# Optimization experiments

Hardware: AMD Instinct MI355X
Metric: run time of the kernel (lower is better)

## Reference

```python
import jax, jax.numpy as jnp
import numpy as np

HEAD_SIZE = 64
EMB_SIZE = 1024
B, T = 8, 2048


def setup_inputs() -> dict:
    key = jax.random.key(0)
    k_x, k_q, k_k, k_v, k_m = jax.random.split(key, 5)
    X = jax.random.normal(k_x, (B, T, EMB_SIZE), dtype=jnp.float32)
    # nn.Linear(emb, head, bias=False) weights have shape (head, emb)
    s = EMB_SIZE ** -0.5
    Wq = jax.random.uniform(k_q, (HEAD_SIZE, EMB_SIZE), jnp.float32, -s, s)
    Wk = jax.random.uniform(k_k, (HEAD_SIZE, EMB_SIZE), jnp.float32, -s, s)
    Wv = jax.random.uniform(k_v, (HEAD_SIZE, EMB_SIZE), jnp.float32, -s, s)
    padding_mask = jax.random.randint(k_m, (B, T), 0, 2).astype(bool)
    # ensure no row is fully masked (would yield NaN softmax)
    padding_mask = padding_mask.at[:, 0].set(False)
    return {"X": X, "Wq": Wq, "Wk": Wk, "Wv": Wv, "padding_mask": padding_mask}


def reference(X, Wq, Wk, Wv, padding_mask):
    # X: (B,T,C); W*: (H,C); padding_mask: (B,T) bool, True = masked key
    C = X.shape[-1]
    Q = jnp.einsum('btc,hc->bth', X, Wq)
    K = jnp.einsum('btc,hc->bth', X, Wk)
    V = jnp.einsum('btc,hc->bth', X, Wv)
    # NOTE: source scales by emb_size**-0.5 (C), not head_size**-0.5
    wei = jnp.einsum('bth,bsh->bts', Q, K) * (C ** -0.5)  # (B,T,T)
    wei = jnp.where(padding_mask[:, None, :], -jnp.inf, wei)
    wei = jax.nn.softmax(wei, axis=-1)  # dropout disabled (eval mode)
    out = jnp.einsum('bts,bsh->bth', wei, V)  # (B,T,H)
    return out
```

## Files before the change

kernel.cpp:

```cpp
#include <hip/hip_runtime.h>
#include <hip/hip_bf16.h>
#include <math.h>


#define T_SEQ 2048
#define EMB 1024
#define HS 64
#define NB 8

typedef __attribute__((ext_vector_type(8))) short short8;
typedef __attribute__((ext_vector_type(4))) float f32x4;
typedef __attribute__((ext_vector_type(2))) unsigned int uint2_t;
typedef unsigned short ushort_t;

static __device__ inline ushort_t f2bf(float f) {
  union { float f; unsigned u; } v; v.f = f;
  unsigned r = v.u + 0x7FFF + ((v.u >> 16) & 1);
  return (ushort_t)(r >> 16);
}
static __device__ inline unsigned pk2(float a, float b) {
  return (unsigned)f2bf(a) | ((unsigned)f2bf(b) << 16);
}
static __device__ inline void lds_barrier() {
  asm volatile("s_waitcnt lgkmcnt(0)" ::: "memory");
  __builtin_amdgcn_s_barrier();
}

__global__ __launch_bounds__(256) void convw_kernel(
    const float* __restrict__ Wq, const float* __restrict__ Wk,
    const float* __restrict__ Wv, ushort_t* __restrict__ Wb) {
  const int m = blockIdx.x >> 4;
  const int blk = blockIdx.x & 15;
  const float* src = (m == 0) ? Wq : (m == 1) ? Wk : Wv;
  const float scale = (m == 0) ? 0.03125f : 1.0f;
  const int base = blk * 4096 + threadIdx.x * 16;
  ushort_t* dst = Wb + m * 65536;
  ushort_t tmp[16];
#pragma unroll
  for (int j = 0; j < 4; ++j) {
    float4 x = *(const float4*)(src + base + j * 4);
    tmp[j * 4 + 0] = f2bf(x.x * scale);
    tmp[j * 4 + 1] = f2bf(x.y * scale);
    tmp[j * 4 + 2] = f2bf(x.z * scale);
    tmp[j * 4 + 3] = f2bf(x.w * scale);
  }
  *(short8*)(dst + base) = *(short8*)tmp;
  *(short8*)(dst + base + 8) = *(short8*)(tmp + 8);
}

__global__ __launch_bounds__(256) void proj_kernel(
    const float* __restrict__ X, const ushort_t* __restrict__ Wb,
    ushort_t* __restrict__ Qb, ushort_t* __restrict__ Kb,
    ushort_t* __restrict__ Vtb) {
  __shared__ __align__(16) ushort_t Xs[2][64 * 128];
  const int tid = threadIdx.x;
  const int lane = tid & 63, w = tid >> 6;
  const int l15 = lane & 15, hi = lane >> 4;
  const long rbase = (long)blockIdx.x * 64;

  const ushort_t* Wrow[3];
#pragma unroll
  for (int t = 0; t < 3; ++t) {
    const int ht = 3 * w + t, m = ht >> 2, hs = ht & 3;
    Wrow[t] = Wb + m * 65536 + (hs * 16 + l15) * 1024 + hi * 8;
  }

  short8 wfA[6], wfB[6], wfC[6], wfD[6];
  auto loadw = [&](short8 (&dst)[6], int s) {
#pragma unroll
    for (int t = 0; t < 3; ++t) {
      dst[2 * t + 0] = *(const short8*)(Wrow[t] + s * 64);
      dst[2 * t + 1] = *(const short8*)(Wrow[t] + s * 64 + 32);
    }
  };
  loadw(wfA, 0); loadw(wfB, 1); loadw(wfC, 2);

  float4 xrA[8], xrB[8];
  auto stage_load = [&](float4 (&xr)[8], int c) {
#pragma unroll
    for (int j = 0; j < 8; ++j) {
      const int F = j * 256 + tid;
      const int row = F >> 5, c4 = F & 31;
      xr[j] = *(const float4*)(X + (rbase + row) * EMB + c * 128 + c4 * 4);
    }
  };
  auto stage_write = [&](float4 (&xr)[8], int buf) {
    ushort_t* Xd = Xs[buf];
#pragma unroll
    for (int j = 0; j < 8; ++j) {
      const int F = j * 256 + tid;
      const int row = F >> 5, c4 = F & 31;
      uint2_t pv;
      pv.x = pk2(xr[j].x, xr[j].y);
      pv.y = pk2(xr[j].z, xr[j].w);
      *(uint2_t*)((char*)(Xd + row * 128) + ((c4 * 8) ^ ((row & 7) << 4))) = pv;
    }
  };

  f32x4 acc[4][3];
#pragma unroll
  for (int rt = 0; rt < 4; ++rt)
#pragma unroll
    for (int t = 0; t < 3; ++t) acc[rt][t] = (f32x4){0.f, 0.f, 0.f, 0.f};

  const int swA = (l15 & 7) << 4;

  auto body = [&](int s, int buf, short8 (&cur)[6], short8 (&pre)[6]) {
    if (s + 3 < 16) loadw(pre, s + 3);
    const int sb = (s & 1) * 128;
#pragma unroll
    for (int rt = 0; rt < 4; ++rt) {
      const char* rowp = (const char*)(Xs[buf] + (rt * 16 + l15) * 128);
      short8 a0 = *(const short8*)(rowp + ((sb + hi * 16) ^ swA));
      short8 a1 = *(const short8*)(rowp + ((sb + 64 + hi * 16) ^ swA));
#pragma unroll
      for (int t = 0; t < 3; ++t) {
        acc[rt][t] = __builtin_amdgcn_mfma_f32_16x16x32_bf16(
            a0, cur[2 * t + 0], acc[rt][t], 0, 0, 0);
        acc[rt][t] = __builtin_amdgcn_mfma_f32_16x16x32_bf16(
            a1, cur[2 * t + 1], acc[rt][t], 0, 0, 0);
      }
    }
  };

  stage_load(xrA, 0);
  stage_write(xrA, 0);
  stage_load(xrB, 1);
  lds_barrier();

  stage_load(xrA, 2);
  body(0, 0, wfA, wfD); body(1, 0, wfB, wfA);
  stage_write(xrB, 1); lds_barrier();
  stage_load(xrB, 3);
  body(2, 1, wfC, wfB); body(3, 1, wfD, wfC);
  stage_write(xrA, 0); lds_barrier();
  stage_load(xrA, 4);
  body(4, 0, wfA, wfD); body(5, 0, wfB, wfA);
  stage_write(xrB, 1); lds_barrier();
  stage_load(xrB, 5);
  body(6, 1, wfC, wfB); body(7, 1, wfD, wfC);
  stage_write(xrA, 0); lds_barrier();
  stage_load(xrA, 6);
  body(8, 0, wfA, wfD); body(9, 0, wfB, wfA);
  stage_write(xrB, 1); lds_barrier();
  stage_load(xrB, 7);
  body(10, 1, wfC, wfB); body(11, 1, wfD, wfC);
  stage_write(xrA, 0); lds_barrier();
  body(12, 0, wfA, wfD); body(13, 0, wfB, wfA);
  stage_write(xrB, 1); lds_barrier();
  body(14, 1, wfC, wfB); body(15, 1, wfD, wfC);

  const long bblk = rbase >> 11;
  const long tb0 = rbase & 2047;
  ushort_t* outs[2] = {Qb, Kb};
#pragma unroll
  for (int rt = 0; rt < 4; ++rt)
#pragma unroll
    for (int t = 0; t < 3; ++t) {
      const int ht = 3 * w + t, m = ht >> 2, hs = ht & 3;
      const int h = hs * 16 + l15;
      if (m < 2) {
#pragma unroll
        for (int r = 0; r < 4; ++r) {
          const long row = rbase + rt * 16 + 4 * hi + r;
          outs[m][row * 64 + h] = f2bf(acc[rt][t][r]);
        }
      } else {
        const long tloc = tb0 + rt * 16 + 4 * hi;
        uint2_t v;
        v.x = pk2(acc[rt][t][0], acc[rt][t][1]);
        v.y = pk2(acc[rt][t][2], acc[rt][t][3]);
        *(uint2_t*)(Vtb + bblk * (long)HS * T_SEQ + (long)h * T_SEQ + tloc) = v;
      }
    }
}

__global__ __launch_bounds__(512) void attn_kernel(
    const ushort_t* __restrict__ Qb, const ushort_t* __restrict__ Kb,
    const ushort_t* __restrict__ Vtb, const int* __restrict__ mask,
    float* __restrict__ out) {
  __shared__ __align__(16) char Lds[152064];

  const int tid = threadIdx.x;
  const int lane = tid & 63, w = tid >> 6;
  const int l15 = lane & 15, hi = lane >> 4;
  const int qs = w & 3, g = w >> 2;
  const int si = tid & 255;
  const int id = blockIdx.x;
  const int b = id & 7;
  const int q0 = (id >> 3) * 64;

  ushort_t* biasB = (ushort_t*)(Lds + 147456);
  float* alphaArr = (float*)(Lds + 151552);

  {
    const ushort_t nb = f2bf(-1e30f);
    const int* mp = mask + b * T_SEQ + tid * 4;
    int4 m0 = *(const int4*)(mp);
    ushort_t t4[4];
    t4[0] = m0.x ? nb : 0; t4[1] = m0.y ? nb : 0;
    t4[2] = m0.z ? nb : 0; t4[3] = m0.w ? nb : 0;
    *(uint2_t*)(biasB + tid * 4) = *(uint2_t*)t4;
  }

  const ushort_t* Qrow = Qb + (long)(b * T_SEQ + q0 + qs * 16 + l15) * 64;
  const short8 qf0 = *(const short8*)(Qrow + hi * 8);
  const short8 qf1 = *(const short8*)(Qrow + 32 + hi * 8);

  const ushort_t* Kg = Kb + (long)b * T_SEQ * 64;
  const ushort_t* Vg = Vtb + (long)b * HS * T_SEQ;

  short8 kregA[2], vregA[2], kregB[2], vregB[2];
  auto stage_load = [&](short8 (&kreg)[2], short8 (&vreg)[2], int t) {
    const ushort_t* ktile = Kg + (g * 1024 + t * 64) * 64;
#pragma unroll
    for (int j = 0; j < 2; ++j)
      kreg[j] = *(const short8*)(ktile + (j * 32 + (si >> 3)) * 64 + (si & 7) * 8);
    const ushort_t* vtile = Vg + (long)(si >> 2) * T_SEQ + g * 1024 + t * 64;
#pragma unroll
    for (int j = 0; j < 2; ++j)
      vreg[j] = *(const short8*)(vtile + (si & 3) * 8 + j * 32);
  };
  auto stage_write = [&](short8 (&kreg)[2], short8 (&vreg)[2], int buf) {
    char* Kd = Lds + (g * 4 + buf) * 8192;
#pragma unroll
    for (int j = 0; j < 2; ++j) {
      const int row = j * 32 + (si >> 3);
      *(short8*)(Kd + row * 128 + (((si & 7) * 16) ^ ((row & 7) << 4))) = kreg[j];
    }
    char* Vd = Lds + 65536 + (g * 4 + buf) * 8192;
    const int vrow = si >> 2, sv = (vrow & 7) << 4;
#pragma unroll
    for (int j = 0; j < 2; ++j)
      *(short8*)(Vd + vrow * 128 + ((((si & 3) * 16) + j * 64) ^ sv)) = vreg[j];
  };

  f32x4 O[4];
#pragma unroll
  for (int ht = 0; ht < 4; ++ht) O[ht] = (f32x4){0.f, 0.f, 0.f, 0.f};
  float mrow = -1e30f, lsum = 0.f;

  char* prow = Lds + 131072 + w * 2048 + l15 * 128;
  const int sw = (l15 & 7) << 4;
  const int swr = (l15 & 7) << 4;

  auto tile_compute = [&](int t, int buf) {
    f32x4 s[4];
    const char* Kl = Lds + (g * 4 + buf) * 8192;
    __builtin_amdgcn_s_setprio(1);
#pragma unroll
    for (int kt = 0; kt < 4; ++kt) {
      const char* kr = Kl + (kt * 16 + l15) * 128;
      short8 k0 = *(const short8*)(kr + ((hi * 16) ^ swr));
      short8 k1 = *(const short8*)(kr + ((64 + hi * 16) ^ swr));
      f32x4 z = {0.f, 0.f, 0.f, 0.f};
      s[kt] = __builtin_amdgcn_mfma_f32_16x16x32_bf16(k0, qf0, z, 0, 0, 0);
      s[kt] = __builtin_amdgcn_mfma_f32_16x16x32_bf16(k1, qf1, s[kt], 0, 0, 0);
    }
    __builtin_amdgcn_s_setprio(0);

    const ushort_t* blp = biasB + g * 1024 + t * 64;
#pragma unroll
    for (int kt = 0; kt < 4; ++kt) {
      const uint2_t bu = *(const uint2_t*)(blp + kt * 16 + hi * 4);
      union { unsigned u; float f; } c0, c1, c2, c3;
      c0.u = bu.x << 16; c1.u = bu.x & 0xFFFF0000u;
      c2.u = bu.y << 16; c3.u = bu.y & 0xFFFF0000u;
      s[kt][0] += c0.f; s[kt][1] += c1.f;
      s[kt][2] += c2.f; s[kt][3] += c3.f;
    }

    float t0m = fmaxf(fmaxf(s[0][0], s[0][1]), fmaxf(s[0][2], s[0][3]));
    float t1m = fmaxf(fmaxf(s[1][0], s[1][1]), fmaxf(s[1][2], s[1][3]));
    float t2m = fmaxf(fmaxf(s[2][0], s[2][1]), fmaxf(s[2][2], s[2][3]));
    float t3m = fmaxf(fmaxf(s[3][0], s[3][1]), fmaxf(s[3][2], s[3][3]));
    float mt = fmaxf(fmaxf(t0m, t1m), fmaxf(t2m, t3m));
    mt = fmaxf(mt, __shfl_xor(mt, 16, 64));
    mt = fmaxf(mt, __shfl_xor(mt, 32, 64));

    const bool skip = __all(mt <= mrow + 8.0f);
    float mnew = mrow;
    if (!skip) {
      mnew = fmaxf(mrow, mt);
      const float alpha = __expf(mrow - mnew);
      if (lane < 16) alphaArr[w * 16 + l15] = alpha;
      lsum *= alpha;
      mrow = mnew;
    }

    float psum = 0.f;
#pragma unroll
    for (int kt = 0; kt < 4; ++kt) {
      const float p0 = __expf(s[kt][0] - mnew);
      const float p1 = __expf(s[kt][1] - mnew);
      const float p2 = __expf(s[kt][2] - mnew);
      const float p3 = __expf(s[kt][3] - mnew);
      psum += (p0 + p1) + (p2 + p3);
      const int a0 = (kt * 32 + hi * 8) ^ sw;
      *(unsigned*)(prow + a0) = pk2(p0, p1);
      *(unsigned*)(prow + a0 + 4) = pk2(p2, p3);
    }
    lsum += psum;

    if (!skip) {
      const f32x4 av = *(const f32x4*)(alphaArr + w * 16 + 4 * hi);
#pragma unroll
      for (int ht = 0; ht < 4; ++ht) O[ht] *= av;
    }

    short8 pa0 = *(const short8*)(prow + ((hi * 16) ^ sw));
    short8 pa1 = *(const short8*)(prow + ((64 + hi * 16) ^ sw));
    const char* Vl = Lds + 65536 + (g * 4 + buf) * 8192;
    __builtin_amdgcn_s_setprio(1);
#pragma unroll
    for (int ht = 0; ht < 4; ++ht) {
      const char* vr = Vl + (ht * 16 + l15) * 128;
      short8 v0 = *(const short8*)(vr + ((hi * 16) ^ swr));
      short8 v1 = *(const short8*)(vr + ((64 + hi * 16) ^ swr));
      O[ht] = __builtin_amdgcn_mfma_f32_16x16x32_bf16(pa0, v0, O[ht], 0, 0, 0);
      O[ht] = __builtin_amdgcn_mfma_f32_16x16x32_bf16(pa1, v1, O[ht], 0, 0, 0);
    }
    __builtin_amdgcn_s_setprio(0);
  };

  stage_load(kregA, vregA, 0);
  stage_load(kregB, vregB, 1);
  stage_write(kregA, vregA, 0);
  stage_write(kregB, vregB, 1);
  lds_barrier();

#pragma unroll 1
  for (int ts = 0; ts < 16; ts += 2) {
    if (ts + 2 < 16) {
      stage_load(kregA, vregA, ts + 2);
      stage_load(kregB, vregB, ts + 3);
    }
    tile_compute(ts, ts & 3);
    tile_compute(ts + 1, (ts + 1) & 3);
    if (ts + 2 < 16) {
      stage_write(kregA, vregA, (ts + 2) & 3);
      stage_write(kregB, vregB, (ts + 3) & 3);
    }
    lds_barrier();
  }

  lsum += __shfl_xor(lsum, 16, 64);
  lsum += __shfl_xor(lsum, 32, 64);

  float* mergeF = (float*)Lds;
  if (g == 1) {
    float* ml = mergeF + (qs * 64 + lane) * 18;
    ml[0] = mrow; ml[1] = lsum;
#pragma unroll
    for (int ht = 0; ht < 4; ++ht)
#pragma unroll
      for (int r = 0; r < 4; ++r) ml[2 + ht * 4 + r] = O[ht][r];
  }
  lds_barrier();
  if (g == 0) {
    const float* ml = mergeF + (qs * 64 + lane) * 18;
    const float mB = ml[0], lB = ml[1];
    const float mn = fmaxf(mrow, mB);
    const float aa = __expf(mrow - mn);
    const float ab = __expf(mB - mn);
    const float inv = 1.0f / (lsum * aa + lB * ab);
    float* ob = out + (long)(b * T_SEQ + q0 + qs * 16) * 64;
#pragma unroll
    for (int r = 0; r < 4; ++r) {
      const float aar = __shfl(aa, 4 * hi + r, 64);
      const float abr = __shfl(ab, 4 * hi + r, 64);
      const float invr = __shfl(inv, 4 * hi + r, 64);
#pragma unroll
      for (int ht = 0; ht < 4; ++ht)
        ob[(4 * hi + r) * 64 + ht * 16 + l15] =
            (O[ht][r] * aar + ml[2 + ht * 4 + r] * abr) * invr;
    }
  }
}

extern "C" void kernel_launch(void* const* d_in, const int* in_sizes, int n_in,
                              void* d_out, int out_size, void* d_ws, size_t ws_size,
                              hipStream_t stream) {
  const float* X  = (const float*)d_in[0];
  const float* Wq = (const float*)d_in[1];
  const float* Wk = (const float*)d_in[2];
  const float* Wv = (const float*)d_in[3];
  const int* mask = (const int*)d_in[4];
  float* outp = (float*)d_out;

  const long NT = (long)NB * T_SEQ * HS;
  ushort_t* wsb = (ushort_t*)d_ws;
  ushort_t* Qb  = wsb;
  ushort_t* Kb  = wsb + NT;
  ushort_t* Vtb = wsb + 2 * NT;
  ushort_t* Wb  = wsb + 3 * NT;

  convw_kernel<<<48, 256, 0, stream>>>(Wq, Wk, Wv, Wb);
  proj_kernel<<<(NB * T_SEQ) / 64, 256, 0, stream>>>(X, Wb, Qb, Kb, Vtb);
  attn_kernel<<<256, 512, 0, stream>>>(Qb, Kb, Vtb, mask, outp);
}
```

Baseline: 54.39 us.

## Stage K/V tiles via direct global-to-LDS loads and use exp2 softmax

Replaces the register-staged K/V tile loads and LDS writes with global_load_lds direct-to-LDS transfers, applying the XOR swizzle on the global address side so the LDS layout is unchanged. This frees VGPRs and removes the separate LDS write pass. Separately, log2(e) is folded into the Q weight scale so the softmax uses exp2f instead of __expf, with the rescale-skip threshold adjusted to match. Barriers become __syncthreads, which relies on the compiler inserting the vmcnt waits the async LDS loads need.

```diff
diff --git a/kernel.cpp b/kernel.cpp
--- a/kernel.cpp
+++ b/kernel.cpp
@@ -25,6 +25,11 @@
   asm volatile("s_waitcnt lgkmcnt(0)" ::: "memory");
   __builtin_amdgcn_s_barrier();
 }
+
+#define GL16(gp, lp)                                                 \
+  __builtin_amdgcn_global_load_lds(                                  \
+      (const __attribute__((address_space(1))) void*)(gp),           \
+      (__attribute__((address_space(3))) void*)(lp), 16, 0, 0)
 
 __global__ __launch_bounds__(256) void convw_kernel(
     const float* __restrict__ Wq, const float* __restrict__ Wk,
@@ -32,7 +37,7 @@
   const int m = blockIdx.x >> 4;
   const int blk = blockIdx.x & 15;
   const float* src = (m == 0) ? Wq : (m == 1) ? Wk : Wv;
-  const float scale = (m == 0) ? 0.03125f : 1.0f;
+  const float scale = (m == 0) ? 0.03125f * 1.44269504f : 1.0f;
   const int base = blk * 4096 + threadIdx.x * 16;
   ushort_t* dst = Wb + m * 65536;
   ushort_t tmp[16];
@@ -210,29 +215,25 @@
   const ushort_t* Kg = Kb + (long)b * T_SEQ * 64;
   const ushort_t* Vg = Vtb + (long)b * HS * T_SEQ;
 
-  short8 kregA[2], vregA[2], kregB[2], vregB[2];
-  auto stage_load = [&](short8 (&kreg)[2], short8 (&vreg)[2], int t) {
+  auto stage_gl = [&](int t, int buf) {
+    char* Kd = Lds + (g * 4 + buf) * 8192;
     const ushort_t* ktile = Kg + (g * 1024 + t * 64) * 64;
 #pragma unroll
-    for (int j = 0; j < 2; ++j)
-      kreg[j] = *(const short8*)(ktile + (j * 32 + (si >> 3)) * 64 + (si & 7) * 8);
-    const ushort_t* vtile = Vg + (long)(si >> 2) * T_SEQ + g * 1024 + t * 64;
-#pragma unroll
-    for (int j = 0; j < 2; ++j)
-      vreg[j] = *(const short8*)(vtile + (si & 3) * 8 + j * 32);
-  };
-  auto stage_write = [&](short8 (&kreg)[2], short8 (&vreg)[2], int buf) {
-    char* Kd = Lds + (g * 4 + buf) * 8192;
-#pragma unroll
     for (int j = 0; j < 2; ++j) {
-      const int row = j * 32 + (si >> 3);
-      *(short8*)(Kd + row * 128 + (((si & 7) * 16) ^ ((row & 7) << 4))) = kreg[j];
+      const int F = j * 256 + si;
+      const int row = F >> 3, sl = F & 7;
+      const int gsl = sl ^ (row & 7);
+      GL16(ktile + row * 64 + gsl * 8, Kd + F * 16);
     }
     char* Vd = Lds + 65536 + (g * 4 + buf) * 8192;
-    const int vrow = si >> 2, sv = (vrow & 7) << 4;
-#pragma unroll
-    for (int j = 0; j < 2; ++j)
-      *(short8*)(Vd + vrow * 128 + ((((si & 3) * 16) + j * 64) ^ sv)) = vreg[j];
+    const ushort_t* vtile = Vg + g * 1024 + t * 64;
+#pragma unroll
+    for (int j = 0; j < 2; ++j) {
+      const int F = j * 256 + si;
+      const int row = F >> 3, sl = F & 7;
+      const int gsl = sl ^ (row & 7);
+      GL16(vtile + (long)row * T_SEQ + gsl * 8, Vd + F * 16);
+    }
   };
 
   f32x4 O[4];
@@ -278,11 +279,11 @@
     mt = fmaxf(mt, __shfl_xor(mt, 16, 64));
     mt = fmaxf(mt, __shfl_xor(mt, 32, 64));
 
-    const bool skip = __all(mt <= mrow + 8.0f);
+    const bool skip = __all(mt <= mrow + 11.5415603f);
     float mnew = mrow;
     if (!skip) {
       mnew = fmaxf(mrow, mt);
-      const float alpha = __expf(mrow - mnew);
+      const float alpha = exp2f(mrow - mnew);
       if (lane < 16) alphaArr[w * 16 + l15] = alpha;
       lsum *= alpha;
       mrow = mnew;
@@ -291,10 +292,10 @@
     float psum = 0.f;
 #pragma unroll
     for (int kt = 0; kt < 4; ++kt) {
-      const float p0 = __expf(s[kt][0] - mnew);
-      const float p1 = __expf(s[kt][1] - mnew);
-      const float p2 = __expf(s[kt][2] - mnew);
-      const float p3 = __expf(s[kt][3] - mnew);
+      const float p0 = exp2f(s[kt][0] - mnew);
+      const float p1 = exp2f(s[kt][1] - mnew);
+      const float p2 = exp2f(s[kt][2] - mnew);
+      const float p3 = exp2f(s[kt][3] - mnew);
       psum += (p0 + p1) + (p2 + p3);
       const int a0 = (kt * 32 + hi * 8) ^ sw;
       *(unsigned*)(prow + a0) = pk2(p0, p1);
@@ -323,25 +324,19 @@
     __builtin_amdgcn_s_setprio(0);
   };
 
-  stage_load(kregA, vregA, 0);
-  stage_load(kregB, vregB, 1);
-  stage_write(kregA, vregA, 0);
-  stage_write(kregB, vregB, 1);
-  lds_barrier();
+  stage_gl(0, 0);
+  stage_gl(1, 1);
+  __syncthreads();
 
 #pragma unroll 1
   for (int ts = 0; ts < 16; ts += 2) {
     if (ts + 2 < 16) {
-      stage_load(kregA, vregA, ts + 2);
-      stage_load(kregB, vregB, ts + 3);
+      stage_gl(ts + 2, (ts + 2) & 3);
+      stage_gl(ts + 3, (ts + 3) & 3);
     }
     tile_compute(ts, ts & 3);
     tile_compute(ts + 1, (ts + 1) & 3);
-    if (ts + 2 < 16) {
-      stage_write(kregA, vregA, (ts + 2) & 3);
-      stage_write(kregB, vregB, (ts + 3) & 3);
-    }
-    lds_barrier();
+    __syncthreads();
   }
 
   lsum += __shfl_xor(lsum, 16, 64);
@@ -356,13 +351,13 @@
 #pragma unroll
       for (int r = 0; r < 4; ++r) ml[2 + ht * 4 + r] = O[ht][r];
   }
-  lds_barrier();
+  __syncthreads();
   if (g == 0) {
     const float* ml = mergeF + (qs * 64 + lane) * 18;
     const float mB = ml[0], lB = ml[1];
     const float mn = fmaxf(mrow, mB);
-    const float aa = __expf(mrow - mn);
-    const float ab = __expf(mB - mn);
+    const float aa = exp2f(mrow - mn);
+    const float ab = exp2f(mB - mn);
     const float inv = 1.0f / (lsum * aa + lB * ab);
     float* ob = out + (long)(b * T_SEQ + q0 + qs * 16) * 64;
 #pragma unroll
```

Measured after the change: 53.94 us (median of 2 runs). Within noise of the previous version (-0.8%).
